# Kernel tuning notes

Measured on AMD Instinct MI355X. Metric: run time of the kernel, lower is better.

## Reference

```python
import jax, jax.numpy as jnp
import numpy as np
from jax import lax

D_MODEL, D_STATE, D_CONV, EXPAND = 64, 16, 4, 2
D_INNER = EXPAND * D_MODEL          # 128
DT_RANK = (D_MODEL + 15) // 16      # 4 = ceil(d_model/16), mamba_ssm 'auto'
B, L, N_IDX = 512, 256, 2048


def setup_inputs() -> dict:
    key = jax.random.key(0)
    ks = jax.random.split(key, 14)
    g = lambda k, shape, s: jax.random.normal(k, shape, jnp.float32) * s
    return {
        "reads": jax.random.normal(ks[0], (B, L, 4), jnp.float32),
        "sequenced_reads_indices": jax.random.randint(ks[1], (N_IDX,), 0, B),
        "exp_w": g(ks[2], (4, D_MODEL), 0.5),
        "exp_b": jnp.zeros((D_MODEL,), jnp.float32),
        "in_proj_w": g(ks[3], (D_MODEL, 2 * D_INNER), 0.1),
        "conv_w": g(ks[4], (D_INNER, 1, D_CONV), 0.3),
        "conv_b": jnp.zeros((D_INNER,), jnp.float32),
        "x_proj_w": g(ks[5], (D_INNER, DT_RANK + 2 * D_STATE), 0.1),
        "dt_w": g(ks[6], (DT_RANK, D_INNER), 0.3),
        "dt_b": jnp.full((D_INNER,), -4.6, jnp.float32),  # softplus(-4.6) ~ 0.01, mamba dt init scale
        "A_log": jnp.log(jnp.broadcast_to(jnp.arange(1, D_STATE + 1, dtype=jnp.float32), (D_INNER, D_STATE))),
        "D_skip": jnp.ones((D_INNER,), jnp.float32),
        "out_proj_w": g(ks[7], (D_INNER, D_MODEL), 0.1),
        "q_w": g(ks[8], (2 * D_MODEL, D_MODEL), 0.1),
        "q_b": jnp.zeros((D_MODEL,), jnp.float32),
        "k_w": g(ks[9], (2 * D_MODEL, D_MODEL), 0.1),
        "k_b": jnp.zeros((D_MODEL,), jnp.float32),
    }


def _mamba(x, in_proj_w, conv_w, conv_b, x_proj_w, dt_w, dt_b, A_log, D_skip, out_proj_w):
    # x: [b, l, d_model]
    xm, z = jnp.split(x @ in_proj_w, 2, axis=-1)  # each [b, l, d_inner]
    # causal depthwise conv over the sequence axis (pad left by d_conv-1, truncate to l)
    xc = lax.conv_general_dilated(
        xm.transpose(0, 2, 1), conv_w, (1,), [(D_CONV - 1, 0)],
        dimension_numbers=("NCH", "OIH", "NCH"), feature_group_count=D_INNER)
    xc = jax.nn.silu(xc + conv_b[None, :, None]).transpose(0, 2, 1)  # [b, l, d_inner]
    dt, Bm, Cm = jnp.split(xc @ x_proj_w, [DT_RANK, DT_RANK + D_STATE], axis=-1)
    delta = jax.nn.softplus(dt @ dt_w + dt_b)  # [b, l, d_inner]
    A = -jnp.exp(A_log)                        # [d_inner, d_state]

    def step(h, inp):
        d_t, B_t, C_t, u_t = inp  # [b,di], [b,ds], [b,ds], [b,di]
        h = jnp.exp(d_t[:, :, None] * A) * h + (d_t * u_t)[:, :, None] * B_t[:, None, :]
        return h, jnp.einsum("bdn,bn->bd", h, C_t)

    h0 = jnp.zeros((x.shape[0], D_INNER, D_STATE), x.dtype)
    xs = (delta.transpose(1, 0, 2), Bm.transpose(1, 0, 2),
          Cm.transpose(1, 0, 2), xc.transpose(1, 0, 2))
    _, ys = lax.scan(jax.checkpoint(step), h0, xs)  # ys: [l, b, d_inner]
    y = ys.transpose(1, 0, 2) + xc * D_skip
    return (y * jax.nn.silu(z)) @ out_proj_w  # [b, l, d_model]


def reference(reads, sequenced_reads_indices, exp_w, exp_b, in_proj_w, conv_w, conv_b,
              x_proj_w, dt_w, dt_b, A_log, D_skip, out_proj_w, q_w, q_b, k_w, k_b):
    x = reads @ exp_w + exp_b  # [b, l, d_model]
    enc = _mamba(x, in_proj_w, conv_w, conv_b, x_proj_w, dt_w, dt_b, A_log, D_skip, out_proj_w)
    mean_pooled = enc.mean(axis=1)        # [b, d_model]
    last_pooled = enc[:, -1, :]           # [b, d_model] (max pool computed in torch but unused)
    pooled = jnp.concatenate([mean_pooled, last_pooled], axis=-1)  # [b, 2*d_model]
    seq = pooled[sequenced_reads_indices]  # [n, 2*d_model]
    queries = seq @ q_w + q_b
    keys = pooled @ k_w + k_b
    return jnp.einsum("nd,md->nm", queries, keys)  # [n, b]
```

## Files before the change

### kernel.cpp

```cpp
#include <hip/hip_runtime.h>
#include <math.h>

#define L_SEQ 256
#define TILE 32

typedef __attribute__((ext_vector_type(2))) float f32x2;
typedef __attribute__((ext_vector_type(4))) float f32x4;
typedef __attribute__((ext_vector_type(8))) _Float16 f16x8;
typedef __attribute__((ext_vector_type(2))) _Float16 f16x2;

__device__ __forceinline__ f32x2 fma2(f32x2 a, f32x2 b, f32x2 c) {
    return __builtin_elementwise_fma(a, b, c);
}
__device__ __forceinline__ f32x2 splat2(float x) { f32x2 v = {x, x}; return v; }
__device__ __forceinline__ float silu_f(float x) { return x / (1.f + __expf(-x)); }
__device__ __forceinline__ float sp2_f(float x) {
    return log2f(1.f + exp2f(x * 1.44269504f)) * 0.69314718f;
}

__global__ __launch_bounds__(256)
void k_prep(const float* __restrict__ exp_w, const float* __restrict__ exp_b,
            const float* __restrict__ in_proj_w, const float* __restrict__ x_proj_w,
            const float* __restrict__ dt_w,
            float* __restrict__ weff, float* __restrict__ beff, _Float16* __restrict__ WT)
{
    const int t = threadIdx.x;
    if (blockIdx.x == 0) {
        float a0 = 0, a1 = 0, a2 = 0, a3 = 0, ab = 0;
        for (int k = 0; k < 64; ++k) {
            float w = in_proj_w[k * 256 + t];
            a0 = fmaf(exp_w[k], w, a0);
            a1 = fmaf(exp_w[64 + k], w, a1);
            a2 = fmaf(exp_w[128 + k], w, a2);
            a3 = fmaf(exp_w[192 + k], w, a3);
            ab = fmaf(exp_b[k], w, ab);
        }
        weff[t] = a0; weff[256 + t] = a1; weff[512 + t] = a2; weff[768 + t] = a3;
        beff[t] = ab;
    } else {
        const int base = (blockIdx.x - 1) * 4096;
        for (int i = base + t; i < base + 4096; i += 256) {
            const int row = i >> 7, k = i & 127;
            float v;
            if (row < 128) {
                v = x_proj_w[k * 36 + 0] * dt_w[row]
                  + x_proj_w[k * 36 + 1] * dt_w[128 + row]
                  + x_proj_w[k * 36 + 2] * dt_w[256 + row]
                  + x_proj_w[k * 36 + 3] * dt_w[384 + row];
            } else {
                v = x_proj_w[k * 36 + 4 + (row - 128)];
            }
            WT[i] = (_Float16)v;
        }
    }
}

template<int NSEG>
__global__ __launch_bounds__(512, 8)
void mamba_seg(const float* __restrict__ reads,
               const float* __restrict__ weff, const float* __restrict__ beff,
               const _Float16* __restrict__ WT,
               const float* __restrict__ conv_w, const float* __restrict__ conv_b,
               const float* __restrict__ dt_b,
               const float* __restrict__ A_log, const float* __restrict__ D_skip,
               f16x2* __restrict__ Qg, f16x2* __restrict__ Pg, f16x2* __restrict__ Kg,
               float* __restrict__ GS, float* __restrict__ CZ, float* __restrict__ SL,
               int Bn)
{
    constexpr int NTILE_ = (L_SEQ / TILE) / NSEG;
    constexpr int NRD = (NTILE_ > 1) ? 2 : 1;
    const int bx = blockIdx.x;
    const int b = bx / NSEG;
    const int sidx = bx - b * NSEG;
    const int seg0 = sidx * NTILE_ * TILE;
    const int t = threadIdx.x;
    const int dA = t & 127, lh = t >> 7;
    const int dd = t >> 2,  g  = t & 3;

    __shared__ __align__(16) float    RD[NRD][36 * 4];
    __shared__ __align__(16) _Float16 XC[TILE * 136];
    __shared__ __align__(16) float    BC[TILE * 32];
    __shared__ _Float16               ZS[TILE * 128];
    __shared__ _Float16               DE[TILE * 128];

    const float dskip = D_skip[dd];
    const float c1 = -1.44269504f * (float)(4 * g + 1);
    bool structured = true;
#pragma unroll
    for (int k = 0; k < 4; ++k) {
        float a = -__expf(A_log[dd * 16 + g * 4 + k]);
        structured = structured && (fabsf(a + (float)(g * 4 + k + 1)) < 1e-3f);
    }

    const float4* rdv = (const float4*)(reads + (size_t)b * L_SEQ * 4);
    if (t < 35) {
        int row = seg0 - 3 + t;
        float4 v = make_float4(0.f, 0.f, 0.f, 0.f);
        if (row >= 0) v = rdv[row];
        ((float4*)RD[0])[t] = v;
    }

    f32x2 h2[2], P2[2], K2[2];
#pragma unroll
    for (int k = 0; k < 2; ++k) { h2[k] = splat2(0.f); P2[k] = splat2(1.f); K2[k] = splat2(0.f); }
    float gsum = 0.f;

    __syncthreads();

    for (int tile = 0; tile < NTILE_; ++tile) {
        const int cur = (NRD > 1) ? (tile & 1) : 0;
        const int l_off = seg0 + tile * TILE;
        const float4* RDc = (const float4*)RD[cur];

        {
            f32x2 wj0 = {weff[dA],       weff[128 + dA]};
            f32x2 wj1 = {weff[256 + dA], weff[384 + dA]};
            f32x2 wj2 = {weff[512 + dA], weff[640 + dA]};
            f32x2 b2  = {beff[dA],       beff[128 + dA]};
            f32x2 wj3 = {weff[768 + dA], weff[896 + dA]};
            const float4 cw = ((const float4*)conv_w)[dA];
            const float cb = conv_b[dA];
            const int lb = lh * 8;
            float x0, x1, x2;
#pragma unroll
            for (int jj = 0; jj < 3; ++jj) {
                float4 rv = RDc[lb + jj];
                f32x2 xz = fma2(splat2(rv.w), wj3, fma2(splat2(rv.z), wj2,
                           fma2(splat2(rv.y), wj1, fma2(splat2(rv.x), wj0, b2))));
                float v = (l_off + lb - 3 + jj >= 0) ? xz.x : 0.f;
                if (jj == 0) x0 = v; else if (jj == 1) x1 = v; else x2 = v;
            }
#pragma unroll
            for (int i = 0; i < 8; ++i) {
                float4 rv = RDc[lb + 3 + i];
                f32x2 xz = fma2(splat2(rv.w), wj3, fma2(splat2(rv.z), wj2,
                           fma2(splat2(rv.y), wj1, fma2(splat2(rv.x), wj0, b2))));
                float s = cb + x0 * cw.x + x1 * cw.y + x2 * cw.z + xz.x * cw.w;
                XC[(lb + i) * 136 + dA] = (_Float16)silu_f(s);
                ZS[(lb + i) * 128 + dA] = (_Float16)silu_f(xz.y);
                x0 = x1; x1 = x2; x2 = xz.x;
            }
        }
        __syncthreads();

        {
            if (NTILE_ > 1 && t < 35 && tile + 1 < NTILE_) {
                int row = l_off + TILE - 3 + t;
                ((float4*)RD[cur ^ 1])[t] = rdv[row];
            }
            const int lane = t & 63;
            const int wv = t >> 6;
            const int fcol = lane & 15;
            const int kq = lane >> 4;
            const int rbase = kq * 4;
#pragma unroll
            for (int i = 0; i < 3; ++i) {
                const int tid = wv + 8 * i;
                if (tid >= 20) break;
                const int m = tid & 1, n = tid >> 1;
                f32x4 acc = {0.f, 0.f, 0.f, 0.f};
#pragma unroll
                for (int ks = 0; ks < 4; ++ks) {
                    const int ko = ks * 32 + kq * 8;
                    f16x8 af = *(const f16x8*)&XC[(m * 16 + fcol) * 136 + ko];
                    f16x8 bf = *(const f16x8*)&WT[(n * 16 + fcol) * 128 + ko];
                    acc = __builtin_amdgcn_mfma_f32_16x16x32_f16(af, bf, acc, 0, 0, 0);
                }
                if (n < 8) {
                    const int ch = n * 16 + fcol;
                    const float db = dt_b[ch];
#pragma unroll
                    for (int r = 0; r < 4; ++r)
                        DE[(m * 16 + rbase + r) * 128 + ch] = (_Float16)sp2_f(acc[r] + db);
                } else {
                    const int jb = (n - 8) * 16 + fcol;
#pragma unroll
                    for (int r = 0; r < 4; ++r)
                        BC[(m * 16 + rbase + r) * 32 + jb] = acc[r];
                }
            }
        }
        __syncthreads();

        {
            auto scan_loop = [&](bool needpk) {
                for (int l = 0; l < TILE; ++l) {
                    const float de = (float)DE[l * 128 + dd];
                    const float zs = (float)ZS[l * 128 + dd];
                    const float xc = (float)XC[l * 136 + dd];
                    const float du = de * xc;
                    f32x2 E2[2];
                    if (structured) {
                        const float r  = exp2f(de * -1.44269504f);
                        const float t1 = exp2f(de * c1);
                        const float r2 = r * r;
                        E2[0] = (f32x2){t1, t1 * r};
                        E2[1] = E2[0] * splat2(r2);
                    } else {
#pragma unroll
                        for (int k = 0; k < 2; ++k) {
                            float e0 = exp2f(de * (-__expf(A_log[dd * 16 + g * 4 + 2 * k])) * 1.44269504f);
                            float e1 = exp2f(de * (-__expf(A_log[dd * 16 + g * 4 + 2 * k + 1])) * 1.44269504f);
                            E2[k] = (f32x2){e0, e1};
                        }
                    }
                    const float4 Bq = *(const float4*)&BC[l * 32 + g * 4];
                    const float4 Cq = *(const float4*)&BC[l * 32 + 16 + g * 4];
                    const f32x2 B2[2] = {{Bq.x, Bq.y}, {Bq.z, Bq.w}};
                    const f32x2 C2[2] = {{Cq.x, Cq.y}, {Cq.z, Cq.w}};
                    const f32x2 dus = splat2(du), zss = splat2(zs);
                    f32x2 yp2 = splat2(0.f);
#pragma unroll
                    for (int k = 0; k < 2; ++k) {
                        h2[k] = fma2(E2[k], h2[k], dus * B2[k]);
                        yp2 = fma2(h2[k], C2[k], yp2);
                        if (needpk) {
                            P2[k] = P2[k] * E2[k];
                            K2[k] = fma2(zss, C2[k] * P2[k], K2[k]);
                        }
                    }
                    float yp = yp2.x + yp2.y;
                    yp += __shfl_xor(yp, 1);
                    yp += __shfl_xor(yp, 2);
                    gsum += fmaf(xc, dskip, yp) * zs;
                }
            };
            if (sidx == 0) scan_loop(false);
            else           scan_loop(true);
        }
        if (NTILE_ > 1) __syncthreads();
    }

    {
        const float zs_last = (float)ZS[(TILE - 1) * 128 + dd];
        const float xc_last = (float)XC[(TILE - 1) * 136 + dd];
        const size_t sb = (size_t)sidx * Bn + b;
#pragma unroll
        for (int k = 0; k < 2; ++k) {
            const size_t o = (sb * 8 + g * 2 + k) * 128 + dd;
            Qg[o] = (f16x2){(_Float16)h2[k].x, (_Float16)h2[k].y};
            if (sidx != 0) {
                Pg[o] = (f16x2){(_Float16)P2[k].x, (_Float16)P2[k].y};
                Kg[o] = (f16x2){(_Float16)K2[k].x, (_Float16)K2[k].y};
            }
        }
        if (g == 0) GS[sb * 128 + dd] = gsum;
        if (sidx == NSEG - 1) {
#pragma unroll
            for (int k = 0; k < 4; ++k)
                CZ[((size_t)b * 16 + g * 4 + k) * 128 + dd] =
                    zs_last * BC[(TILE - 1) * 32 + 16 + g * 4 + k];
            if (g == 0) SL[(size_t)b * 128 + dd] = zs_last * xc_last * dskip;
        }
    }
}

template<int NS>
__global__ __launch_bounds__(128)
void stitch(const f16x2* __restrict__ Qg, const f16x2* __restrict__ Pg,
            const f16x2* __restrict__ Kg, const float* __restrict__ GS,
            const float* __restrict__ CZ, const float* __restrict__ SL,
            const float* __restrict__ out_proj_w,
            const float* __restrict__ k_w, const float* __restrict__ k_b,
            float* __restrict__ pooled, float* __restrict__ keysT,
            int Bn)
{
    const int b = blockIdx.x, d = threadIdx.x;
    __shared__ float gb[256];
    __shared__ float pl[128];

    float h[16];
    float gsum = GS[(size_t)b * 128 + d];
#pragma unroll
    for (int p = 0; p < 8; ++p) {
        f16x2 q = Qg[((size_t)b * 8 + p) * 128 + d];
        h[2 * p] = (float)q[0]; h[2 * p + 1] = (float)q[1];
    }
#pragma unroll
    for (int s = 1; s < NS; ++s) {
        const size_t sb = (size_t)s * Bn + b;
        gsum += GS[sb * 128 + d];
        float corr = 0.f;
#pragma unroll
        for (int p = 0; p < 8; ++p) {
            const size_t o = (sb * 8 + p) * 128 + d;
            f16x2 qv = Qg[o], pv = Pg[o], kv = Kg[o];
            corr = fmaf((float)kv[0], h[2 * p], corr);
            corr = fmaf((float)kv[1], h[2 * p + 1], corr);
            h[2 * p]     = fmaf((float)pv[0], h[2 * p],     (float)qv[0]);
            h[2 * p + 1] = fmaf((float)pv[1], h[2 * p + 1], (float)qv[1]);
        }
        gsum += corr;
    }
    float glast = SL[(size_t)b * 128 + d];
#pragma unroll
    for (int n = 0; n < 16; ++n)
        glast = fmaf(CZ[((size_t)b * 16 + n) * 128 + d], h[n], glast);

    gb[d] = gsum * (1.f / (float)L_SEQ);
    gb[128 + d] = glast;
    __syncthreads();
    {
        const int half = d >> 6, oc = d & 63;
        const float* gbp = &gb[half * 128];
        float s = 0.f;
#pragma unroll 16
        for (int i = 0; i < 128; ++i) s = fmaf(gbp[i], out_proj_w[i * 64 + oc], s);
        pooled[(size_t)b * 128 + d] = s;
        pl[d] = s;
    }
    __syncthreads();
    if (d < 64) {
        float s = k_b[d];
#pragma unroll 16
        for (int i = 0; i < 128; ++i) s = fmaf(pl[i], k_w[i * 64 + d], s);
        keysT[(size_t)d * Bn + b] = s;
    }
}

__global__ __launch_bounds__(128)
void qk_kernel(const float* __restrict__ pooled, const int* __restrict__ idx,
               const float* __restrict__ q_w, const float* __restrict__ q_b,
               const float* __restrict__ keysT, float* __restrict__ out, int B)
{
    const int n = blockIdx.x, t = threadIdx.x;
    __shared__ float p_lds[128];
    __shared__ float q_lds[64];
    const int bi = idx[n];
    p_lds[t] = pooled[(size_t)bi * 128 + t];
    __syncthreads();
    if (t < 64) {
        float s = q_b[t];
#pragma unroll
        for (int i = 0; i < 128; ++i) s = fmaf(p_lds[i], q_w[i * 64 + t], s);
        q_lds[t] = s;
    }
    __syncthreads();
    f32x4 acc = {0.f, 0.f, 0.f, 0.f};
    const int m0 = t * 4;
#pragma unroll 8
    for (int i = 0; i < 64; ++i) {
        const float qi = q_lds[i];
        const float4 kv = *(const float4*)&keysT[(size_t)i * B + m0];
        acc[0] = fmaf(qi, kv.x, acc[0]);
        acc[1] = fmaf(qi, kv.y, acc[1]);
        acc[2] = fmaf(qi, kv.z, acc[2]);
        acc[3] = fmaf(qi, kv.w, acc[3]);
    }
    *(f32x4*)&out[(size_t)n * B + m0] = acc;
}


extern "C" void kernel_launch(void* const* d_in, const int* in_sizes, int n_in,
                              void* d_out, int out_size, void* d_ws, size_t ws_size,
                              hipStream_t stream)
{
    const float* reads      = (const float*)d_in[0];
    const int*   idx        = (const int*)d_in[1];
    const float* exp_w      = (const float*)d_in[2];
    const float* exp_b      = (const float*)d_in[3];
    const float* in_proj_w  = (const float*)d_in[4];
    const float* conv_w     = (const float*)d_in[5];
    const float* conv_b     = (const float*)d_in[6];
    const float* x_proj_w   = (const float*)d_in[7];
    const float* dt_w       = (const float*)d_in[8];
    const float* dt_b       = (const float*)d_in[9];
    const float* A_log      = (const float*)d_in[10];
    const float* D_skip     = (const float*)d_in[11];
    const float* out_proj_w = (const float*)d_in[12];
    const float* q_w        = (const float*)d_in[13];
    const float* q_b        = (const float*)d_in[14];
    const float* k_w        = (const float*)d_in[15];
    const float* k_b        = (const float*)d_in[16];

    const int B = in_sizes[0] / (L_SEQ * 4);
    const int N = in_sizes[1];

    char* wsb = (char*)d_ws;
    size_t off = 0;
    auto alloc = [&](size_t bytes) {
        size_t o = off;
        off = (off + bytes + 255) & ~(size_t)255;
        return o;
    };

    float*     pooled = (float*)(wsb + alloc((size_t)B * 128 * 4));
    float*     keysT  = (float*)(wsb + alloc((size_t)B * 64 * 4));
    float*     weff   = (float*)(wsb + alloc(1024 * 4));
    float*     beff   = (float*)(wsb + alloc(256 * 4));
    _Float16*  WT     = (_Float16*)(wsb + alloc(160 * 128 * 2));

    auto summ_bytes = [&](int nseg) {
        size_t pairs = (size_t)B * nseg * 8 * 128;
        return pairs * 4 * 3
             + (size_t)B * nseg * 128 * 4
             + (size_t)B * 16 * 128 * 4
             + (size_t)B * 128 * 4 + 8192;
    };
    const int nseg = (off + summ_bytes(8) <= ws_size) ? 8 : 1;

    const size_t pairs = (size_t)B * nseg * 8 * 128;
    f16x2* Qg = (f16x2*)(wsb + alloc(pairs * 4));
    f16x2* Pg = (f16x2*)(wsb + alloc(pairs * 4));
    f16x2* Kg = (f16x2*)(wsb + alloc(pairs * 4));
    float* GS = (float*)(wsb + alloc((size_t)B * nseg * 128 * 4));
    float* CZ = (float*)(wsb + alloc((size_t)B * 16 * 128 * 4));
    float* SL = (float*)(wsb + alloc((size_t)B * 128 * 4));

    k_prep<<<6, 256, 0, stream>>>(exp_w, exp_b, in_proj_w, x_proj_w, dt_w,
                                  weff, beff, WT);
    if (nseg == 8) {
        mamba_seg<8><<<B * 8, 512, 0, stream>>>(reads, weff, beff, WT,
                                                conv_w, conv_b, dt_b, A_log, D_skip,
                                                Qg, Pg, Kg, GS, CZ, SL, B);
        stitch<8><<<B, 128, 0, stream>>>(Qg, Pg, Kg, GS, CZ, SL, out_proj_w, k_w, k_b,
                                         pooled, keysT, B);
    } else {
        mamba_seg<1><<<B, 512, 0, stream>>>(reads, weff, beff, WT,
                                            conv_w, conv_b, dt_b, A_log, D_skip,
                                            Qg, Pg, Kg, GS, CZ, SL, B);
        stitch<1><<<B, 128, 0, stream>>>(Qg, Pg, Kg, GS, CZ, SL, out_proj_w, k_w, k_b,
                                         pooled, keysT, B);
    }
    qk_kernel<<<N, 128, 0, stream>>>(pooled, idx, q_w, q_b, keysT, (float*)d_out, B);
}
```

Measured before the change: 144.1 us.

## Fold input projection and causal conv into one MFMA GEMM, halve scan threads

Precomputes a combined weight matrix W2 that folds the expansion, in_proj and the depthwise causal conv taps into a single 32-wide K dimension. Each tile then builds a small fp16 feature matrix of shifted reads plus validity flags and produces XC and ZS with one 16x16x32 MFMA per output tile, replacing the per-thread scalar FMA and conv code. The scan now uses 256 threads, each holding 8 states instead of 4, which removes one shuffle per step but leaves half the block idle during the scan. The launch-bounds occupancy hint drops from 8 to 6, the reads double-buffer prefetch is removed, and the prep kernel is split into two launches. The reads and weights are now rounded to fp16 before the conv, which costs some precision.

```diff
diff --git a/kernel.cpp b/kernel.cpp
--- a/kernel.cpp
+++ b/kernel.cpp
@@ -19,26 +19,34 @@
 }
 
 __global__ __launch_bounds__(256)
-void k_prep(const float* __restrict__ exp_w, const float* __restrict__ exp_b,
-            const float* __restrict__ in_proj_w, const float* __restrict__ x_proj_w,
-            const float* __restrict__ dt_w,
-            float* __restrict__ weff, float* __restrict__ beff, _Float16* __restrict__ WT)
+void k_prep1(const float* __restrict__ exp_w, const float* __restrict__ exp_b,
+             const float* __restrict__ in_proj_w,
+             float* __restrict__ weff, float* __restrict__ beff)
 {
     const int t = threadIdx.x;
-    if (blockIdx.x == 0) {
-        float a0 = 0, a1 = 0, a2 = 0, a3 = 0, ab = 0;
-        for (int k = 0; k < 64; ++k) {
-            float w = in_proj_w[k * 256 + t];
-            a0 = fmaf(exp_w[k], w, a0);
-            a1 = fmaf(exp_w[64 + k], w, a1);
-            a2 = fmaf(exp_w[128 + k], w, a2);
-            a3 = fmaf(exp_w[192 + k], w, a3);
-            ab = fmaf(exp_b[k], w, ab);
-        }
-        weff[t] = a0; weff[256 + t] = a1; weff[512 + t] = a2; weff[768 + t] = a3;
-        beff[t] = ab;
-    } else {
-        const int base = (blockIdx.x - 1) * 4096;
+    float a0 = 0, a1 = 0, a2 = 0, a3 = 0, ab = 0;
+    for (int k = 0; k < 64; ++k) {
+        float w = in_proj_w[k * 256 + t];
+        a0 = fmaf(exp_w[k], w, a0);
+        a1 = fmaf(exp_w[64 + k], w, a1);
+        a2 = fmaf(exp_w[128 + k], w, a2);
+        a3 = fmaf(exp_w[192 + k], w, a3);
+        ab = fmaf(exp_b[k], w, ab);
+    }
+    weff[t] = a0; weff[256 + t] = a1; weff[512 + t] = a2; weff[768 + t] = a3;
+    beff[t] = ab;
+}
+
+__global__ __launch_bounds__(256)
+void k_prep2(const float* __restrict__ x_proj_w, const float* __restrict__ dt_w,
+             const float* __restrict__ conv_w, const float* __restrict__ conv_b,
+             const float* __restrict__ weff, const float* __restrict__ beff,
+             _Float16* __restrict__ WT, _Float16* __restrict__ W2, float* __restrict__ bias2)
+{
+    const int t = threadIdx.x;
+    const int blk = blockIdx.x;
+    if (blk < 5) {
+        const int base = blk * 4096;
         for (int i = base + t; i < base + 4096; i += 256) {
             const int row = i >> 7, k = i & 127;
             float v;
@@ -52,107 +60,113 @@
             }
             WT[i] = (_Float16)v;
         }
+    } else if (blk == 5) {
+        for (int i = t; i < 128 * 32; i += 256) {
+            const int d = i >> 5, j = i & 31;
+            float v = 0.f;
+            if (j < 16)      v = conv_w[d * 4 + (j >> 2)] * weff[(j & 3) * 256 + d];
+            else if (j < 20) v = conv_w[d * 4 + (j - 16)] * beff[d];
+            W2[i] = (_Float16)v;
+        }
+        if (t < 128) bias2[t] = conv_b[t];
+    } else {
+        for (int i = t; i < 128 * 32; i += 256) {
+            const int d = i >> 5, j = i & 31;
+            float v = 0.f;
+            if (j >= 12 && j < 16) v = weff[(j - 12) * 256 + 128 + d];
+            else if (j == 19)      v = beff[128 + d];
+            W2[128 * 32 + i] = (_Float16)v;
+        }
     }
 }
 
 template<int NSEG>
-__global__ __launch_bounds__(512, 8)
+__global__ __launch_bounds__(512, 6)
 void mamba_seg(const float* __restrict__ reads,
-               const float* __restrict__ weff, const float* __restrict__ beff,
-               const _Float16* __restrict__ WT,
-               const float* __restrict__ conv_w, const float* __restrict__ conv_b,
-               const float* __restrict__ dt_b,
+               const _Float16* __restrict__ WT, const _Float16* __restrict__ W2,
+               const float* __restrict__ bias2, const float* __restrict__ dt_b,
                const float* __restrict__ A_log, const float* __restrict__ D_skip,
                f16x2* __restrict__ Qg, f16x2* __restrict__ Pg, f16x2* __restrict__ Kg,
                float* __restrict__ GS, float* __restrict__ CZ, float* __restrict__ SL,
                int Bn)
 {
     constexpr int NTILE_ = (L_SEQ / TILE) / NSEG;
-    constexpr int NRD = (NTILE_ > 1) ? 2 : 1;
     const int bx = blockIdx.x;
     const int b = bx / NSEG;
     const int sidx = bx - b * NSEG;
     const int seg0 = sidx * NTILE_ * TILE;
     const int t = threadIdx.x;
-    const int dA = t & 127, lh = t >> 7;
-    const int dd = t >> 2,  g  = t & 3;
-
-    __shared__ __align__(16) float    RD[NRD][36 * 4];
+    const int dd = t >> 1, g = t & 1;
+
+    __shared__ __align__(16) _Float16 F[32 * 40];
     __shared__ __align__(16) _Float16 XC[TILE * 136];
     __shared__ __align__(16) float    BC[TILE * 32];
     __shared__ _Float16               ZS[TILE * 128];
     __shared__ _Float16               DE[TILE * 128];
 
-    const float dskip = D_skip[dd];
-    const float c1 = -1.44269504f * (float)(4 * g + 1);
+    float dskip = 0.f, c1 = 0.f;
     bool structured = true;
-#pragma unroll
-    for (int k = 0; k < 4; ++k) {
-        float a = -__expf(A_log[dd * 16 + g * 4 + k]);
-        structured = structured && (fabsf(a + (float)(g * 4 + k + 1)) < 1e-3f);
-    }
-
-    const float4* rdv = (const float4*)(reads + (size_t)b * L_SEQ * 4);
-    if (t < 35) {
-        int row = seg0 - 3 + t;
-        float4 v = make_float4(0.f, 0.f, 0.f, 0.f);
-        if (row >= 0) v = rdv[row];
-        ((float4*)RD[0])[t] = v;
-    }
-
-    f32x2 h2[2], P2[2], K2[2];
-#pragma unroll
-    for (int k = 0; k < 2; ++k) { h2[k] = splat2(0.f); P2[k] = splat2(1.f); K2[k] = splat2(0.f); }
+    if (t < 256) {
+        dskip = D_skip[dd];
+        c1 = -1.44269504f * (float)(8 * g + 1);
+#pragma unroll
+        for (int k = 0; k < 8; ++k) {
+            float a = -__expf(A_log[dd * 16 + g * 8 + k]);
+            structured = structured && (fabsf(a + (float)(g * 8 + k + 1)) < 1e-3f);
+        }
+    }
+
+    f32x2 h2[4], P2[4], K2[4];
+#pragma unroll
+    for (int k = 0; k < 4; ++k) { h2[k] = splat2(0.f); P2[k] = splat2(1.f); K2[k] = splat2(0.f); }
     float gsum = 0.f;
 
-    __syncthreads();
-
     for (int tile = 0; tile < NTILE_; ++tile) {
-        const int cur = (NRD > 1) ? (tile & 1) : 0;
         const int l_off = seg0 + tile * TILE;
-        const float4* RDc = (const float4*)RD[cur];
+
+        for (int i = t; i < 32 * 40; i += 512) {
+            const int l = i / 40, j = i - l * 40;
+            _Float16 v = (_Float16)0.f;
+            if (j < 16) {
+                const int row = l_off + l - 3 + (j >> 2);
+                if (row >= 0) v = (_Float16)reads[((size_t)b * L_SEQ + row) * 4 + (j & 3)];
+            } else if (j < 20) {
+                v = (l_off + l - 3 + (j - 16) >= 0) ? (_Float16)1.f : (_Float16)0.f;
+            }
+            F[i] = v;
+        }
+        __syncthreads();
 
         {
-            f32x2 wj0 = {weff[dA],       weff[128 + dA]};
-            f32x2 wj1 = {weff[256 + dA], weff[384 + dA]};
-            f32x2 wj2 = {weff[512 + dA], weff[640 + dA]};
-            f32x2 b2  = {beff[dA],       beff[128 + dA]};
-            f32x2 wj3 = {weff[768 + dA], weff[896 + dA]};
-            const float4 cw = ((const float4*)conv_w)[dA];
-            const float cb = conv_b[dA];
-            const int lb = lh * 8;
-            float x0, x1, x2;
-#pragma unroll
-            for (int jj = 0; jj < 3; ++jj) {
-                float4 rv = RDc[lb + jj];
-                f32x2 xz = fma2(splat2(rv.w), wj3, fma2(splat2(rv.z), wj2,
-                           fma2(splat2(rv.y), wj1, fma2(splat2(rv.x), wj0, b2))));
-                float v = (l_off + lb - 3 + jj >= 0) ? xz.x : 0.f;
-                if (jj == 0) x0 = v; else if (jj == 1) x1 = v; else x2 = v;
+            const int lane = t & 63, wv = t >> 6;
+            const int fcol = lane & 15, kq = lane >> 4, rbase = kq * 4;
+#pragma unroll
+            for (int i = 0; i < 4; ++i) {
+                const int tid = wv + 8 * i;
+                const int m = tid & 1, n = tid >> 1;
+                f16x8 af = *(const f16x8*)&F[(m * 16 + fcol) * 40 + kq * 8];
+                f16x8 bf = *(const f16x8*)&W2[(n * 16 + fcol) * 32 + kq * 8];
+                f32x4 acc = {0.f, 0.f, 0.f, 0.f};
+                acc = __builtin_amdgcn_mfma_f32_16x16x32_f16(af, bf, acc, 0, 0, 0);
+                if (n < 8) {
+                    const int ch = n * 16 + fcol;
+                    const float bv = bias2[ch];
+#pragma unroll
+                    for (int r = 0; r < 4; ++r)
+                        XC[(m * 16 + rbase + r) * 136 + ch] = (_Float16)silu_f(acc[r] + bv);
+                } else {
+                    const int ch = (n - 8) * 16 + fcol;
+#pragma unroll
+                    for (int r = 0; r < 4; ++r)
+                        ZS[(m * 16 + rbase + r) * 128 + ch] = (_Float16)silu_f(acc[r]);
+                }
             }
-#pragma unroll
-            for (int i = 0; i < 8; ++i) {
-                float4 rv = RDc[lb + 3 + i];
-                f32x2 xz = fma2(splat2(rv.w), wj3, fma2(splat2(rv.z), wj2,
-                           fma2(splat2(rv.y), wj1, fma2(splat2(rv.x), wj0, b2))));
-                float s = cb + x0 * cw.x + x1 * cw.y + x2 * cw.z + xz.x * cw.w;
-                XC[(lb + i) * 136 + dA] = (_Float16)silu_f(s);
-                ZS[(lb + i) * 128 + dA] = (_Float16)silu_f(xz.y);
-                x0 = x1; x1 = x2; x2 = xz.x;
-            }
         }
         __syncthreads();
 
         {
-            if (NTILE_ > 1 && t < 35 && tile + 1 < NTILE_) {
-                int row = l_off + TILE - 3 + t;
-                ((float4*)RD[cur ^ 1])[t] = rdv[row];
-            }
-            const int lane = t & 63;
-            const int wv = t >> 6;
-            const int fcol = lane & 15;
-            const int kq = lane >> 4;
-            const int rbase = kq * 4;
+            const int lane = t & 63, wv = t >> 6;
+            const int fcol = lane & 15, kq = lane >> 4, rbase = kq * 4;
 #pragma unroll
             for (int i = 0; i < 3; ++i) {
                 const int tid = wv + 8 * i;
@@ -182,36 +196,41 @@
         }
         __syncthreads();
 
-        {
+        if (t < 256) {
             auto scan_loop = [&](bool needpk) {
                 for (int l = 0; l < TILE; ++l) {
                     const float de = (float)DE[l * 128 + dd];
                     const float zs = (float)ZS[l * 128 + dd];
                     const float xc = (float)XC[l * 136 + dd];
                     const float du = de * xc;
-                    f32x2 E2[2];
+                    f32x2 E2[4];
                     if (structured) {
-                        const float r  = exp2f(de * -1.44269504f);
+                        const float r = exp2f(de * -1.44269504f);
                         const float t1 = exp2f(de * c1);
                         const float r2 = r * r;
                         E2[0] = (f32x2){t1, t1 * r};
-                        E2[1] = E2[0] * splat2(r2);
+                        const f32x2 r2s = splat2(r2);
+                        E2[1] = E2[0] * r2s;
+                        E2[2] = E2[1] * r2s;
+                        E2[3] = E2[2] * r2s;
                     } else {
 #pragma unroll
-                        for (int k = 0; k < 2; ++k) {
-                            float e0 = exp2f(de * (-__expf(A_log[dd * 16 + g * 4 + 2 * k])) * 1.44269504f);
-                            float e1 = exp2f(de * (-__expf(A_log[dd * 16 + g * 4 + 2 * k + 1])) * 1.44269504f);
+                        for (int k = 0; k < 4; ++k) {
+                            float e0 = exp2f(de * (-__expf(A_log[dd * 16 + g * 8 + 2 * k])) * 1.44269504f);
+                            float e1 = exp2f(de * (-__expf(A_log[dd * 16 + g * 8 + 2 * k + 1])) * 1.44269504f);
                             E2[k] = (f32x2){e0, e1};
                         }
                     }
-                    const float4 Bq = *(const float4*)&BC[l * 32 + g * 4];
-                    const float4 Cq = *(const float4*)&BC[l * 32 + 16 + g * 4];
-                    const f32x2 B2[2] = {{Bq.x, Bq.y}, {Bq.z, Bq.w}};
-                    const f32x2 C2[2] = {{Cq.x, Cq.y}, {Cq.z, Cq.w}};
+                    const float4 Bq0 = *(const float4*)&BC[l * 32 + g * 8];
+                    const float4 Bq1 = *(const float4*)&BC[l * 32 + g * 8 + 4];
+                    const float4 Cq0 = *(const float4*)&BC[l * 32 + 16 + g * 8];
+                    const float4 Cq1 = *(const float4*)&BC[l * 32 + 16 + g * 8 + 4];
+                    const f32x2 B2[4] = {{Bq0.x, Bq0.y}, {Bq0.z, Bq0.w}, {Bq1.x, Bq1.y}, {Bq1.z, Bq1.w}};
+                    const f32x2 C2[4] = {{Cq0.x, Cq0.y}, {Cq0.z, Cq0.w}, {Cq1.x, Cq1.y}, {Cq1.z, Cq1.w}};
                     const f32x2 dus = splat2(du), zss = splat2(zs);
                     f32x2 yp2 = splat2(0.f);
 #pragma unroll
-                    for (int k = 0; k < 2; ++k) {
+                    for (int k = 0; k < 4; ++k) {
                         h2[k] = fma2(E2[k], h2[k], dus * B2[k]);
                         yp2 = fma2(h2[k], C2[k], yp2);
                         if (needpk) {
@@ -220,9 +239,8 @@
                         }
                     }
                     float yp = yp2.x + yp2.y;
-                    yp += __shfl_xor(yp, 1);
-                    yp += __shfl_xor(yp, 2);
-                    gsum += fmaf(xc, dskip, yp) * zs;
+                    const float y = yp + __shfl_xor(yp, 1);
+                    gsum += fmaf(xc, dskip, y) * zs;
                 }
             };
             if (sidx == 0) scan_loop(false);
@@ -231,13 +249,13 @@
         if (NTILE_ > 1) __syncthreads();
     }
 
-    {
+    if (t < 256) {
         const float zs_last = (float)ZS[(TILE - 1) * 128 + dd];
         const float xc_last = (float)XC[(TILE - 1) * 136 + dd];
         const size_t sb = (size_t)sidx * Bn + b;
 #pragma unroll
-        for (int k = 0; k < 2; ++k) {
-            const size_t o = (sb * 8 + g * 2 + k) * 128 + dd;
+        for (int k = 0; k < 4; ++k) {
+            const size_t o = (sb * 8 + g * 4 + k) * 128 + dd;
             Qg[o] = (f16x2){(_Float16)h2[k].x, (_Float16)h2[k].y};
             if (sidx != 0) {
                 Pg[o] = (f16x2){(_Float16)P2[k].x, (_Float16)P2[k].y};
@@ -247,9 +265,9 @@
         if (g == 0) GS[sb * 128 + dd] = gsum;
         if (sidx == NSEG - 1) {
 #pragma unroll
-            for (int k = 0; k < 4; ++k)
-                CZ[((size_t)b * 16 + g * 4 + k) * 128 + dd] =
-                    zs_last * BC[(TILE - 1) * 32 + 16 + g * 4 + k];
+            for (int k = 0; k < 8; ++k)
+                CZ[((size_t)b * 16 + g * 8 + k) * 128 + dd] =
+                    zs_last * BC[(TILE - 1) * 32 + 16 + g * 8 + k];
             if (g == 0) SL[(size_t)b * 128 + dd] = zs_last * xc_last * dskip;
         }
     }
@@ -389,6 +407,8 @@
     float*     weff   = (float*)(wsb + alloc(1024 * 4));
     float*     beff   = (float*)(wsb + alloc(256 * 4));
     _Float16*  WT     = (_Float16*)(wsb + alloc(160 * 128 * 2));
+    _Float16*  W2     = (_Float16*)(wsb + alloc(256 * 32 * 2));
+    float*     bias2  = (float*)(wsb + alloc(128 * 4));
 
     auto summ_bytes = [&](int nseg) {
         size_t pairs = (size_t)B * nseg * 8 * 128;
@@ -407,17 +427,18 @@
     float* CZ = (float*)(wsb + alloc((size_t)B * 16 * 128 * 4));
     float* SL = (float*)(wsb + alloc((size_t)B * 128 * 4));
 
-    k_prep<<<6, 256, 0, stream>>>(exp_w, exp_b, in_proj_w, x_proj_w, dt_w,
-                                  weff, beff, WT);
+    k_prep1<<<1, 256, 0, stream>>>(exp_w, exp_b, in_proj_w, weff, beff);
+    k_prep2<<<7, 256, 0, stream>>>(x_proj_w, dt_w, conv_w, conv_b, weff, beff,
+                                   WT, W2, bias2);
     if (nseg == 8) {
-        mamba_seg<8><<<B * 8, 512, 0, stream>>>(reads, weff, beff, WT,
-                                                conv_w, conv_b, dt_b, A_log, D_skip,
+        mamba_seg<8><<<B * 8, 512, 0, stream>>>(reads, WT, W2, bias2, dt_b,
+                                                A_log, D_skip,
                                                 Qg, Pg, Kg, GS, CZ, SL, B);
         stitch<8><<<B, 128, 0, stream>>>(Qg, Pg, Kg, GS, CZ, SL, out_proj_w, k_w, k_b,
                                          pooled, keysT, B);
     } else {
-        mamba_seg<1><<<B, 512, 0, stream>>>(reads, weff, beff, WT,
-                                            conv_w, conv_b, dt_b, A_log, D_skip,
+        mamba_seg<1><<<B, 512, 0, stream>>>(reads, WT, W2, bias2, dt_b,
+                                            A_log, D_skip,
                                             Qg, Pg, Kg, GS, CZ, SL, B);
         stitch<1><<<B, 128, 0, stream>>>(Qg, Pg, Kg, GS, CZ, SL, out_proj_w, k_w, k_b,
                                          pooled, keysT, B);
```

New measurement: 140.9 us. 1.02x faster.
